# Optimization experiments

Measured on AMD Instinct MI355X. Metric: run time of the kernel, lower is better.

## Reference

```python
import jax, jax.numpy as jnp
import numpy as np

K = 20          # number of NAG iterations (init kwarg k)
MU = 0.05       # strong-convexity constant mu (init kwarg, fixed so no eigendecomp)
B, N = 4096, 128


def setup_inputs() -> dict:
    key = jax.random.key(0)
    k1, k2 = jax.random.split(key)
    w = jax.random.normal(k1, (B, N, N), dtype=jnp.float32)
    b = jax.random.normal(k2, (B, N), dtype=jnp.float32)
    s = jnp.asarray(1e-3, dtype=jnp.float32)  # learned step-size Parameter
    return {"w": w, "b": b, "s": s}


def reference(w, b, s):
    # NAG.forward with mu fixed, x_init=y_init=None (zeros), return_all=False.
    mu = jnp.asarray(MU, dtype=s.dtype)
    sqms = jnp.sqrt(mu * s)
    alpha = (1.0 - sqms) / (1.0 + sqms)  # scalar momentum coefficient

    x0 = jnp.zeros_like(b)
    y0 = jnp.zeros_like(b)

    def step(carry, _):
        x, y = carry
        # GD.gradient_decent(s, y, w, b): x_next = y - s * (w @ y - b)
        grad = jnp.einsum('bij,bj->bi', w, y) - b
        x_next = y - s * grad
        y_new = (1.0 + alpha) * x_next - alpha * x
        return (x_next, y_new), None

    (x, y), _ = jax.lax.scan(step, (x0, y0), None, length=K)
    return (x, y)
```

## Files before the change

kernel.cpp:

```cpp
#include <hip/hip_runtime.h>

#define K_ITERS 20
#define MU_CONST 0.05f
#define BN 128
#define NB 8
#define NBLOCKS 512
#define YSTRIDE 24

typedef float v4f __attribute__((ext_vector_type(4)));
typedef __attribute__((address_space(1))) const v4f gc4;
typedef __attribute__((address_space(1))) v4f g4;

template <int CTRL>
__device__ __forceinline__ float dpp_add(float v) {
    int x = __builtin_amdgcn_update_dpp(0, __float_as_int(v), CTRL, 0xF, 0xF, true);
    return v + __int_as_float(x);
}
__device__ __forceinline__ float reduce8(float v) {
    v = dpp_add<0xB1>(v);
    v = dpp_add<0x4E>(v);
    v = dpp_add<0x141>(v);
    return v;
}

__global__ __launch_bounds__(256, 2) void nag_kernel(
    const float* __restrict__ w,
    const float* __restrict__ bvec,
    const float* __restrict__ s_ptr,
    float* __restrict__ out,
    int B)
{
    __shared__ __align__(16) float y_lds[2][8 * YSTRIDE];

    const int t  = threadIdx.x;
    const int wv = t >> 6;
    const int q  = (t >> 3) & 7;
    const int g  = t & 7;
    const int row0   = wv * 32 + q * 4;
    const int wslice = (row0 >> 4) * YSTRIDE + (q & 3) * 4;
    const int rbase  = g * YSTRIDE;

    const float s     = *s_ptr;
    const float sqms  = sqrtf(MU_CONST * s);
    const float alpha = (1.0f - sqms) / (1.0f + sqms);
    const float ap1   = 1.0f + alpha;

    const int base = blockIdx.x * NB;

    v4f wa[4][4], wb[4][4];
    v4f ba, bbuf;

    auto load_w = [&](v4f (&wr)[4][4], int nb_) {
        const gc4* wp = (const gc4*)(w + (size_t)nb_ * (BN * BN)
                                       + (size_t)row0 * BN + g * 16);
#pragma unroll
        for (int rho = 0; rho < 4; ++rho)
#pragma unroll
            for (int k = 0; k < 4; ++k)
                wr[rho][k] = wp[rho * 32 + k];
    };
    auto load_b = [&](v4f& br, int nb_) {
        br = *(const gc4*)(bvec + (size_t)nb_ * BN + row0);
    };

    auto body = [&](v4f (&wc)[4][4], v4f (&wn)[4][4],
                    v4f& brc, v4f& brn, int batch, bool pf) {
        const float br0 = brc.x, br1 = brc.y, br2 = brc.z, br3 = brc.w;

        float xs[4], ys[4];
        xs[0] = s * br0; xs[1] = s * br1; xs[2] = s * br2; xs[3] = s * br3;
#pragma unroll
        for (int rho = 0; rho < 4; ++rho) ys[rho] = ap1 * xs[rho];
        if (g == 0)
            *reinterpret_cast<v4f*>(&y_lds[0][wslice]) =
                (v4f){ys[0], ys[1], ys[2], ys[3]};

        if (pf) { load_w(wn, batch + 1); load_b(brn, batch + 1); }

        __builtin_amdgcn_sched_barrier(0);
        asm volatile("s_waitcnt lgkmcnt(0)");
        __builtin_amdgcn_s_barrier();
        __builtin_amdgcn_sched_barrier(0);

#pragma unroll 2
        for (int it = 1; it < K_ITERS; ++it) {
            const float* yb = &y_lds[(it + 1) & 1][rbase];
            v4f yv[4];
#pragma unroll
            for (int k = 0; k < 4; ++k)
                yv[k] = *reinterpret_cast<const v4f*>(yb + k * 4);

            float br_[4] = {br0, br1, br2, br3};
#pragma unroll
            for (int rho = 0; rho < 4; ++rho) {
                float p = wc[rho][0].x * yv[0].x;
                p = fmaf(wc[rho][0].y, yv[0].y, p);
                p = fmaf(wc[rho][0].z, yv[0].z, p);
                p = fmaf(wc[rho][0].w, yv[0].w, p);
                p = fmaf(wc[rho][1].x, yv[1].x, p);
                p = fmaf(wc[rho][1].y, yv[1].y, p);
                p = fmaf(wc[rho][1].z, yv[1].z, p);
                p = fmaf(wc[rho][1].w, yv[1].w, p);
                p = fmaf(wc[rho][2].x, yv[2].x, p);
                p = fmaf(wc[rho][2].y, yv[2].y, p);
                p = fmaf(wc[rho][2].z, yv[2].z, p);
                p = fmaf(wc[rho][2].w, yv[2].w, p);
                p = fmaf(wc[rho][3].x, yv[3].x, p);
                p = fmaf(wc[rho][3].y, yv[3].y, p);
                p = fmaf(wc[rho][3].z, yv[3].z, p);
                p = fmaf(wc[rho][3].w, yv[3].w, p);
                const float d  = reduce8(p);
                const float xn = fmaf(-s, d - br_[rho], ys[rho]);
                ys[rho] = fmaf(ap1, xn, -(alpha * xs[rho]));
                xs[rho] = xn;
            }

            if (it != K_ITERS - 1 && g == 0)
                *reinterpret_cast<v4f*>(&y_lds[it & 1][wslice]) =
                    (v4f){ys[0], ys[1], ys[2], ys[3]};

            __builtin_amdgcn_sched_barrier(0);
            asm volatile("s_waitcnt lgkmcnt(0)");
            __builtin_amdgcn_s_barrier();
            __builtin_amdgcn_sched_barrier(0);
        }

        const size_t ob = (size_t)batch * BN + row0;
        if (g == 0)
            *(g4*)(out + ob) = (v4f){xs[0], xs[1], xs[2], xs[3]};
        else if (g == 1)
            *(g4*)(out + (size_t)B * BN + ob) = (v4f){ys[0], ys[1], ys[2], ys[3]};
    };

    load_w(wa, base);
    load_b(ba, base);
#pragma unroll 1
    for (int i2 = 0; i2 < NB / 2; ++i2) {
        body(wa, wb, ba, bbuf, base + 2 * i2, true);
        body(wb, wa, bbuf, ba, base + 2 * i2 + 1, (2 * i2 + 2) < NB);
    }
}

extern "C" void kernel_launch(void* const* d_in, const int* in_sizes, int n_in,
                              void* d_out, int out_size, void* d_ws, size_t ws_size,
                              hipStream_t stream) {
    const float* w = (const float*)d_in[0];
    const float* b = (const float*)d_in[1];
    const float* s = (const float*)d_in[2];
    float* out = (float*)d_out;
    const int B = in_sizes[1] / BN;
    nag_kernel<<<dim3(NBLOCKS), dim3(256), 0, stream>>>(w, b, s, out, B);
}
```

Before: 74.99 us.

## Stage next batch's W via async global_load_lds spread across iterations

Replaces the register double-buffer for the next batch's 128x128 W matrix with asynchronous global->LDS direct loads (64KB swizzled LDS buffer). One chunk is issued per NAG iteration, and after each batch the data is copied from LDS into registers. This halves W register usage and spreads global traffic across the iteration loop, aiming to hide load latency and relieve register pressure. In exchange it adds 64KB of LDS per block, which may limit occupancy below the launch bound of 2 blocks per CU, plus extra barriers and an LDS-to-register copy per batch.

```diff
diff --git a/kernel.cpp b/kernel.cpp
--- a/kernel.cpp
+++ b/kernel.cpp
@@ -10,6 +10,8 @@
 typedef float v4f __attribute__((ext_vector_type(4)));
 typedef __attribute__((address_space(1))) const v4f gc4;
 typedef __attribute__((address_space(1))) v4f g4;
+typedef const __attribute__((address_space(1))) void* gas_ptr;
+typedef __attribute__((address_space(3))) void* las_ptr;
 
 template <int CTRL>
 __device__ __forceinline__ float dpp_add(float v) {
@@ -30,12 +32,14 @@
     float* __restrict__ out,
     int B)
 {
+    __shared__ __align__(16) float lds_w[BN * BN];
     __shared__ __align__(16) float y_lds[2][8 * YSTRIDE];
 
-    const int t  = threadIdx.x;
-    const int wv = t >> 6;
-    const int q  = (t >> 3) & 7;
-    const int g  = t & 7;
+    const int t    = threadIdx.x;
+    const int lane = t & 63;
+    const int wv   = t >> 6;
+    const int q    = (t >> 3) & 7;
+    const int g    = t & 7;
     const int row0   = wv * 32 + q * 4;
     const int wslice = (row0 >> 4) * YSTRIDE + (q & 3) * 4;
     const int rbase  = g * YSTRIDE;
@@ -47,25 +51,37 @@
 
     const int base = blockIdx.x * NB;
 
-    v4f wa[4][4], wb[4][4];
+    v4f w4[4][4];
     v4f ba, bbuf;
+    const v4f* lw4 = (const v4f*)lds_w;
 
-    auto load_w = [&](v4f (&wr)[4][4], int nb_) {
-        const gc4* wp = (const gc4*)(w + (size_t)nb_ * (BN * BN)
-                                       + (size_t)row0 * BN + g * 16);
+    auto stage_chunk = [&](const float* wb, int cc) {
+        const int inst = wv * 16 + cc;
+        const int rho  = inst * 2 + (lane >> 5);
+        const int c4   = lane & 31;
+        const int G    = rho * 32 + (c4 ^ (rho & 7));
+        __builtin_amdgcn_global_load_lds((gas_ptr)(wb + (size_t)G * 4),
+                                         (las_ptr)(lds_w + inst * 256), 16, 0, 0);
+    };
+
+    auto copy_regs = [&]() {
 #pragma unroll
-        for (int rho = 0; rho < 4; ++rho)
+        for (int rr = 0; rr < 4; ++rr) {
+            const int rho = row0 + rr;
+            const int sw  = rho & 7;
 #pragma unroll
             for (int k = 0; k < 4; ++k)
-                wr[rho][k] = wp[rho * 32 + k];
+                w4[rr][k] = lw4[rho * 32 + ((g * 4 + k) ^ sw)];
+        }
     };
+
     auto load_b = [&](v4f& br, int nb_) {
         br = *(const gc4*)(bvec + (size_t)nb_ * BN + row0);
     };
 
-    auto body = [&](v4f (&wc)[4][4], v4f (&wn)[4][4],
-                    v4f& brc, v4f& brn, int batch, bool pf) {
+    auto body = [&](v4f& brc, v4f& brn, int batch, bool pf) {
         const float br0 = brc.x, br1 = brc.y, br2 = brc.z, br3 = brc.w;
+        const float* wbn = w + (size_t)(batch + 1) * (BN * BN);
 
         float xs[4], ys[4];
         xs[0] = s * br0; xs[1] = s * br1; xs[2] = s * br2; xs[3] = s * br3;
@@ -75,7 +91,7 @@
             *reinterpret_cast<v4f*>(&y_lds[0][wslice]) =
                 (v4f){ys[0], ys[1], ys[2], ys[3]};
 
-        if (pf) { load_w(wn, batch + 1); load_b(brn, batch + 1); }
+        if (pf) load_b(brn, batch + 1);
 
         __builtin_amdgcn_sched_barrier(0);
         asm volatile("s_waitcnt lgkmcnt(0)");
@@ -90,25 +106,27 @@
             for (int k = 0; k < 4; ++k)
                 yv[k] = *reinterpret_cast<const v4f*>(yb + k * 4);
 
+            if (pf && it <= 16) stage_chunk(wbn, it - 1);
+
             float br_[4] = {br0, br1, br2, br3};
 #pragma unroll
             for (int rho = 0; rho < 4; ++rho) {
-                float p = wc[rho][0].x * yv[0].x;
-                p = fmaf(wc[rho][0].y, yv[0].y, p);
-                p = fmaf(wc[rho][0].z, yv[0].z, p);
-                p = fmaf(wc[rho][0].w, yv[0].w, p);
-                p = fmaf(wc[rho][1].x, yv[1].x, p);
-                p = fmaf(wc[rho][1].y, yv[1].y, p);
-                p = fmaf(wc[rho][1].z, yv[1].z, p);
-                p = fmaf(wc[rho][1].w, yv[1].w, p);
-                p = fmaf(wc[rho][2].x, yv[2].x, p);
-                p = fmaf(wc[rho][2].y, yv[2].y, p);
-                p = fmaf(wc[rho][2].z, yv[2].z, p);
-                p = fmaf(wc[rho][2].w, yv[2].w, p);
-                p = fmaf(wc[rho][3].x, yv[3].x, p);
-                p = fmaf(wc[rho][3].y, yv[3].y, p);
-                p = fmaf(wc[rho][3].z, yv[3].z, p);
-                p = fmaf(wc[rho][3].w, yv[3].w, p);
+                float p = w4[rho][0].x * yv[0].x;
+                p = fmaf(w4[rho][0].y, yv[0].y, p);
+                p = fmaf(w4[rho][0].z, yv[0].z, p);
+                p = fmaf(w4[rho][0].w, yv[0].w, p);
+                p = fmaf(w4[rho][1].x, yv[1].x, p);
+                p = fmaf(w4[rho][1].y, yv[1].y, p);
+                p = fmaf(w4[rho][1].z, yv[1].z, p);
+                p = fmaf(w4[rho][1].w, yv[1].w, p);
+                p = fmaf(w4[rho][2].x, yv[2].x, p);
+                p = fmaf(w4[rho][2].y, yv[2].y, p);
+                p = fmaf(w4[rho][2].z, yv[2].z, p);
+                p = fmaf(w4[rho][2].w, yv[2].w, p);
+                p = fmaf(w4[rho][3].x, yv[3].x, p);
+                p = fmaf(w4[rho][3].y, yv[3].y, p);
+                p = fmaf(w4[rho][3].z, yv[3].z, p);
+                p = fmaf(w4[rho][3].w, yv[3].w, p);
                 const float d  = reduce8(p);
                 const float xn = fmaf(-s, d - br_[rho], ys[rho]);
                 ys[rho] = fmaf(ap1, xn, -(alpha * xs[rho]));
@@ -130,14 +148,40 @@
             *(g4*)(out + ob) = (v4f){xs[0], xs[1], xs[2], xs[3]};
         else if (g == 1)
             *(g4*)(out + (size_t)B * BN + ob) = (v4f){ys[0], ys[1], ys[2], ys[3]};
+
+        if (pf) {
+            __builtin_amdgcn_sched_barrier(0);
+            asm volatile("s_waitcnt vmcnt(0)");
+            __builtin_amdgcn_s_barrier();
+            __builtin_amdgcn_sched_barrier(0);
+            copy_regs();
+            __builtin_amdgcn_sched_barrier(0);
+            asm volatile("s_waitcnt lgkmcnt(0)");
+            __builtin_amdgcn_s_barrier();
+            __builtin_amdgcn_sched_barrier(0);
+        }
     };
 
-    load_w(wa, base);
     load_b(ba, base);
+    {
+        const float* wb0 = w + (size_t)base * (BN * BN);
+#pragma unroll
+        for (int cc = 0; cc < 16; ++cc) stage_chunk(wb0, cc);
+    }
+    __builtin_amdgcn_sched_barrier(0);
+    asm volatile("s_waitcnt vmcnt(0)");
+    __builtin_amdgcn_s_barrier();
+    __builtin_amdgcn_sched_barrier(0);
+    copy_regs();
+    __builtin_amdgcn_sched_barrier(0);
+    asm volatile("s_waitcnt lgkmcnt(0)");
+    __builtin_amdgcn_s_barrier();
+    __builtin_amdgcn_sched_barrier(0);
+
 #pragma unroll 1
     for (int i2 = 0; i2 < NB / 2; ++i2) {
-        body(wa, wb, ba, bbuf, base + 2 * i2, true);
-        body(wb, wa, bbuf, ba, base + 2 * i2 + 1, (2 * i2 + 2) < NB);
+        body(ba, bbuf, base + 2 * i2, true);
+        body(bbuf, ba, base + 2 * i2 + 1, (2 * i2 + 2) < NB);
     }
 }
 
```

Result: slower. 90.25 us (+20.3%).

## Launch one block per batch instead of persistent blocks with register prefetch

Applied to the files above, without the earlier changes.

Replaces the persistent 512-block design, where each block processed 8 batches and double-buffered the next batch's W in registers, with one block per batch (4096 blocks). Launch bounds are raised to 4 blocks per CU so more blocks can be resident and latency is hidden by occupancy rather than explicit prefetch. The custom waitcnt/s_barrier sequence is replaced by __syncthreads. This drops the second register buffer, but the W load for each block is no longer overlapped with the previous batch's iterations inside the block.

```diff
diff --git a/kernel.cpp b/kernel.cpp
--- a/kernel.cpp
+++ b/kernel.cpp
@@ -3,8 +3,6 @@
 #define K_ITERS 20
 #define MU_CONST 0.05f
 #define BN 128
-#define NB 8
-#define NBLOCKS 512
 #define YSTRIDE 24
 
 typedef float v4f __attribute__((ext_vector_type(4)));
@@ -23,7 +21,7 @@
     return v;
 }
 
-__global__ __launch_bounds__(256, 2) void nag_kernel(
+__global__ __launch_bounds__(256, 4) void nag_kernel(
     const float* __restrict__ w,
     const float* __restrict__ bvec,
     const float* __restrict__ s_ptr,
@@ -40,105 +38,79 @@
     const int wslice = (row0 >> 4) * YSTRIDE + (q & 3) * 4;
     const int rbase  = g * YSTRIDE;
 
+    const int batch = blockIdx.x;
+
+    v4f w4[4][4];
+    const gc4* wp = (const gc4*)(w + (size_t)batch * (BN * BN)
+                                   + (size_t)row0 * BN + g * 16);
+#pragma unroll
+    for (int rho = 0; rho < 4; ++rho)
+#pragma unroll
+        for (int k = 0; k < 4; ++k)
+            w4[rho][k] = wp[rho * 32 + k];
+
+    const v4f br4 = *(const gc4*)(bvec + (size_t)batch * BN + row0);
+    const float br_[4] = {br4.x, br4.y, br4.z, br4.w};
+
     const float s     = *s_ptr;
     const float sqms  = sqrtf(MU_CONST * s);
     const float alpha = (1.0f - sqms) / (1.0f + sqms);
     const float ap1   = 1.0f + alpha;
 
-    const int base = blockIdx.x * NB;
-
-    v4f wa[4][4], wb[4][4];
-    v4f ba, bbuf;
-
-    auto load_w = [&](v4f (&wr)[4][4], int nb_) {
-        const gc4* wp = (const gc4*)(w + (size_t)nb_ * (BN * BN)
-                                       + (size_t)row0 * BN + g * 16);
+    float xs[4], ys[4];
 #pragma unroll
-        for (int rho = 0; rho < 4; ++rho)
-#pragma unroll
-            for (int k = 0; k < 4; ++k)
-                wr[rho][k] = wp[rho * 32 + k];
-    };
-    auto load_b = [&](v4f& br, int nb_) {
-        br = *(const gc4*)(bvec + (size_t)nb_ * BN + row0);
-    };
-
-    auto body = [&](v4f (&wc)[4][4], v4f (&wn)[4][4],
-                    v4f& brc, v4f& brn, int batch, bool pf) {
-        const float br0 = brc.x, br1 = brc.y, br2 = brc.z, br3 = brc.w;
-
-        float xs[4], ys[4];
-        xs[0] = s * br0; xs[1] = s * br1; xs[2] = s * br2; xs[3] = s * br3;
-#pragma unroll
-        for (int rho = 0; rho < 4; ++rho) ys[rho] = ap1 * xs[rho];
-        if (g == 0)
-            *reinterpret_cast<v4f*>(&y_lds[0][wslice]) =
-                (v4f){ys[0], ys[1], ys[2], ys[3]};
-
-        if (pf) { load_w(wn, batch + 1); load_b(brn, batch + 1); }
-
-        __builtin_amdgcn_sched_barrier(0);
-        asm volatile("s_waitcnt lgkmcnt(0)");
-        __builtin_amdgcn_s_barrier();
-        __builtin_amdgcn_sched_barrier(0);
+    for (int rho = 0; rho < 4; ++rho) {
+        xs[rho] = s * br_[rho];
+        ys[rho] = ap1 * xs[rho];
+    }
+    if (g == 0)
+        *reinterpret_cast<v4f*>(&y_lds[0][wslice]) =
+            (v4f){ys[0], ys[1], ys[2], ys[3]};
+    __syncthreads();
 
 #pragma unroll 2
-        for (int it = 1; it < K_ITERS; ++it) {
-            const float* yb = &y_lds[(it + 1) & 1][rbase];
-            v4f yv[4];
+    for (int it = 1; it < K_ITERS; ++it) {
+        const float* yb = &y_lds[(it + 1) & 1][rbase];
+        v4f yv[4];
 #pragma unroll
-            for (int k = 0; k < 4; ++k)
-                yv[k] = *reinterpret_cast<const v4f*>(yb + k * 4);
+        for (int k = 0; k < 4; ++k)
+            yv[k] = *reinterpret_cast<const v4f*>(yb + k * 4);
 
-            float br_[4] = {br0, br1, br2, br3};
 #pragma unroll
-            for (int rho = 0; rho < 4; ++rho) {
-                float p = wc[rho][0].x * yv[0].x;
-                p = fmaf(wc[rho][0].y, yv[0].y, p);
-                p = fmaf(wc[rho][0].z, yv[0].z, p);
-                p = fmaf(wc[rho][0].w, yv[0].w, p);
-                p = fmaf(wc[rho][1].x, yv[1].x, p);
-                p = fmaf(wc[rho][1].y, yv[1].y, p);
-                p = fmaf(wc[rho][1].z, yv[1].z, p);
-                p = fmaf(wc[rho][1].w, yv[1].w, p);
-                p = fmaf(wc[rho][2].x, yv[2].x, p);
-                p = fmaf(wc[rho][2].y, yv[2].y, p);
-                p = fmaf(wc[rho][2].z, yv[2].z, p);
-                p = fmaf(wc[rho][2].w, yv[2].w, p);
-                p = fmaf(wc[rho][3].x, yv[3].x, p);
-                p = fmaf(wc[rho][3].y, yv[3].y, p);
-                p = fmaf(wc[rho][3].z, yv[3].z, p);
-                p = fmaf(wc[rho][3].w, yv[3].w, p);
-                const float d  = reduce8(p);
-                const float xn = fmaf(-s, d - br_[rho], ys[rho]);
-                ys[rho] = fmaf(ap1, xn, -(alpha * xs[rho]));
-                xs[rho] = xn;
-            }
-
-            if (it != K_ITERS - 1 && g == 0)
-                *reinterpret_cast<v4f*>(&y_lds[it & 1][wslice]) =
-                    (v4f){ys[0], ys[1], ys[2], ys[3]};
-
-            __builtin_amdgcn_sched_barrier(0);
-            asm volatile("s_waitcnt lgkmcnt(0)");
-            __builtin_amdgcn_s_barrier();
-            __builtin_amdgcn_sched_barrier(0);
+        for (int rho = 0; rho < 4; ++rho) {
+            float p = w4[rho][0].x * yv[0].x;
+            p = fmaf(w4[rho][0].y, yv[0].y, p);
+            p = fmaf(w4[rho][0].z, yv[0].z, p);
+            p = fmaf(w4[rho][0].w, yv[0].w, p);
+            p = fmaf(w4[rho][1].x, yv[1].x, p);
+            p = fmaf(w4[rho][1].y, yv[1].y, p);
+            p = fmaf(w4[rho][1].z, yv[1].z, p);
+            p = fmaf(w4[rho][1].w, yv[1].w, p);
+            p = fmaf(w4[rho][2].x, yv[2].x, p);
+            p = fmaf(w4[rho][2].y, yv[2].y, p);
+            p = fmaf(w4[rho][2].z, yv[2].z, p);
+            p = fmaf(w4[rho][2].w, yv[2].w, p);
+            p = fmaf(w4[rho][3].x, yv[3].x, p);
+            p = fmaf(w4[rho][3].y, yv[3].y, p);
+            p = fmaf(w4[rho][3].z, yv[3].z, p);
+            p = fmaf(w4[rho][3].w, yv[3].w, p);
+            const float d  = reduce8(p);
+            const float xn = fmaf(-s, d - br_[rho], ys[rho]);
+            ys[rho] = fmaf(ap1, xn, -(alpha * xs[rho]));
+            xs[rho] = xn;
         }
 
-        const size_t ob = (size_t)batch * BN + row0;
-        if (g == 0)
-            *(g4*)(out + ob) = (v4f){xs[0], xs[1], xs[2], xs[3]};
-        else if (g == 1)
-            *(g4*)(out + (size_t)B * BN + ob) = (v4f){ys[0], ys[1], ys[2], ys[3]};
-    };
+        if (it != K_ITERS - 1 && g == 0)
+            *reinterpret_cast<v4f*>(&y_lds[it & 1][wslice]) =
+                (v4f){ys[0], ys[1], ys[2], ys[3]};
+        __syncthreads();
+    }
 
-    load_w(wa, base);
-    load_b(ba, base);
-#pragma unroll 1
-    for (int i2 = 0; i2 < NB / 2; ++i2) {
-        body(wa, wb, ba, bbuf, base + 2 * i2, true);
-        body(wb, wa, bbuf, ba, base + 2 * i2 + 1, (2 * i2 + 2) < NB);
-    }
+    const size_t ob = (size_t)batch * BN + row0;
+    if (g == 0)
+        *(g4*)(out + ob) = (v4f){xs[0], xs[1], xs[2], xs[3]};
+    else if (g == 1)
+        *(g4*)(out + (size_t)B * BN + ob) = (v4f){ys[0], ys[1], ys[2], ys[3]};
 }
 
 extern "C" void kernel_launch(void* const* d_in, const int* in_sizes, int n_in,
@@ -149,5 +121,5 @@
     const float* s = (const float*)d_in[2];
     float* out = (float*)d_out;
     const int B = in_sizes[1] / BN;
-    nag_kernel<<<dim3(NBLOCKS), dim3(256), 0, stream>>>(w, b, s, out, B);
+    nag_kernel<<<dim3(B), dim3(256), 0, stream>>>(w, b, s, out, B);
 }
```

Result: faster. 60.67 us (-19.1%).
